# Optimization experiments

Measured on AMD Instinct MI355X. Metric: run time of the kernel, lower is better.

The kernel has to match this reference:

```python
import jax, jax.numpy as jnp
import numpy as np

N = 50000
E = 400000
IN_DIM = 16
EMB = 32
HID = 128
HEADS = 4
LAYERS = 3
EPS_BN = 1e-5
NEG_SLOPE = 0.2


def setup_inputs() -> dict:
    key = jax.random.key(0)
    ks = jax.random.split(key, 16)
    s = 0.1
    C = HID  # per-head out channels (concat=False)
    inp = {
        "x": jax.random.normal(ks[0], (N, IN_DIM), jnp.float32),
        "edge_index": jax.random.randint(ks[1], (2, E), 0, N, jnp.int64),
        "emb": s * jax.random.normal(ks[2], (N, EMB), jnp.float32),
        "Wf": s * jax.random.normal(ks[3], (EMB, IN_DIM), jnp.float32),
        "bf": jnp.zeros((EMB,), jnp.float32),
        "Wc": s * jax.random.normal(ks[4], (HID, 2 * EMB), jnp.float32),
        "bc": jnp.zeros((HID,), jnp.float32),
        "Wl": s * jax.random.normal(ks[5], (LAYERS, HEADS * C, HID), jnp.float32),
        "a_src": s * jax.random.normal(ks[6], (LAYERS, HEADS, C), jnp.float32),
        "a_dst": s * jax.random.normal(ks[7], (LAYERS, HEADS, C), jnp.float32),
        "bl": jnp.zeros((LAYERS, C), jnp.float32),
        "gamma": jnp.ones((LAYERS, C), jnp.float32),
        "beta": jnp.zeros((LAYERS, C), jnp.float32),
        "Wout": s * jax.random.normal(ks[8], (1, HID), jnp.float32),
        "bout": jnp.zeros((1,), jnp.float32),
    }
    return inp


def _gat_layer(h, src, dst, W, a_s, a_d, b):
    n = h.shape[0]
    C = W.shape[0] // HEADS
    hp = (h @ W.T).reshape(n, HEADS, C)                # (N,H,C)
    al_s = jnp.sum(hp * a_s, axis=-1)                  # (N,H)
    al_d = jnp.sum(hp * a_d, axis=-1)                  # (N,H)
    e = jax.nn.leaky_relu(al_s[src] + al_d[dst], NEG_SLOPE)  # (E,H)
    m = jax.ops.segment_max(e, dst, num_segments=n)    # per-target max
    ex = jnp.exp(e - m[dst])
    denom = jax.ops.segment_sum(ex, dst, num_segments=n) + 1e-16
    alpha = ex / denom[dst]                            # (E,H)
    msg = hp[src] * alpha[..., None]                   # (E,H,C)
    out = jax.ops.segment_sum(msg, dst, num_segments=n)
    return jnp.mean(out, axis=1) + b                   # concat=False: head mean


def _bn(x, g, b):
    mu = jnp.mean(x, axis=0)
    var = jnp.var(x, axis=0)  # biased, as torch BN uses for normalization
    return (x - mu) * jax.lax.rsqrt(var + EPS_BN) * g + b


def reference(x, edge_index, emb, Wf, bf, Wc, bc, Wl, a_src, a_dst, bl, gamma, beta, Wout, bout):
    n = x.shape[0]
    loop = jnp.arange(n, dtype=edge_index.dtype)
    src = jnp.concatenate([edge_index[0], loop])       # add self loops
    dst = jnp.concatenate([edge_index[1], loop])
    feat = x @ Wf.T + bf
    h = jax.nn.relu(jnp.concatenate([emb, feat], axis=1) @ Wc.T + bc)
    prev_h = h
    for i in range(LAYERS):
        h = _gat_layer(h, src, dst, Wl[i], a_src[i], a_dst[i], bl[i])
        h = jax.nn.relu(_bn(h, gamma[i], beta[i]))
        if prev_h.shape == h.shape:
            h = h + prev_h
        prev_h = h
    out = h @ Wout.T + bout
    return jnp.clip(out, -10.0, 10.0)
```

## Files before the change

kernel.cpp:

```cpp
#include <hip/hip_runtime.h>
#include <hip/hip_bf16.h>
#include <math.h>

#define INDIM 16
#define EMBD 32
#define UDIM 64
#define HIDD 128
#define HEADS 4
#define LAYERS 3
#define MPAD 50048
#define NSLICE 32

typedef short v8s __attribute__((ext_vector_type(8)));
typedef float v4f __attribute__((ext_vector_type(4)));

__device__ __forceinline__ float lrelu(float x) { return x > 0.f ? x : 0.2f * x; }
__device__ __forceinline__ float bf2f(unsigned int bits16) {
    unsigned int u = bits16 << 16;
    return __builtin_bit_cast(float, u);
}
__device__ __forceinline__ unsigned short f2bf(float f) {
    unsigned int u = __builtin_bit_cast(unsigned int, f);
    unsigned int lsb = (u >> 16) & 1;
    u += 0x7fff + lsb;
    return (unsigned short)(u >> 16);
}

__global__ __launch_bounds__(256) void k_enc(const float* __restrict__ x,
                                             const float* __restrict__ emb,
                                             const float* __restrict__ Wf,
                                             const float* __restrict__ bf,
                                             unsigned short* __restrict__ u, int n) {
    int i = blockIdx.x * 256 + threadIdx.x;
    if (i >= n * EMBD) return;
    int node = i >> 5, j = i & 31;
    const float* xr = x + (size_t)node * INDIM;
    const float* wr = Wf + (size_t)j * INDIM;
    float s = bf[j];
#pragma unroll
    for (int k = 0; k < INDIM; k++) s += xr[k] * wr[k];
    u[(size_t)node * UDIM + EMBD + j] = f2bf(s);
    u[(size_t)node * UDIM + j] = f2bf(emb[(size_t)node * EMBD + j]);
}

__global__ __launch_bounds__(256) void k_prep_v(const float* __restrict__ Wl,
                                                unsigned short* __restrict__ Vb) {
    int i = blockIdx.x * 256 + threadIdx.x;
    if (i >= LAYERS * HIDD * 512) return;
    int l = i >> 16;
    int rem = i & 65535;
    int c = rem >> 9;
    int f = rem & 511;
    int h = f >> 7, k = f & 127;
    Vb[i] = f2bf(Wl[(size_t)l * 512 * HIDD + (size_t)(h * HIDD + c) * HIDD + k]);
}

__global__ __launch_bounds__(256) void k_prep_a(const float* __restrict__ Wl,
                                                const float* __restrict__ a_s,
                                                const float* __restrict__ a_d,
                                                float* __restrict__ ws, float* __restrict__ wd) {
    int i = blockIdx.x * 256 + threadIdx.x;
    if (i >= LAYERS * HEADS * HIDD) return;
    int l = i >> 9, h = (i >> 7) & 3, k = i & 127;
    const float* W = Wl + (size_t)l * 512 * HIDD;
    const float* as = a_s + l * 512 + h * HIDD;
    const float* ad = a_d + l * 512 + h * HIDD;
    float ss = 0.f, sd = 0.f;
    for (int c = 0; c < HIDD; c++) {
        float w = W[(size_t)(h * HIDD + c) * HIDD + k];
        ss += as[c] * w;
        sd += ad[c] * w;
    }
    ws[i] = ss;
    wd[i] = sd;
}

__global__ __launch_bounds__(256) void k_prep_wc(const float* __restrict__ Wc,
                                                 unsigned short* __restrict__ Wcb) {
    int i = blockIdx.x * 256 + threadIdx.x;
    if (i < HIDD * UDIM) Wcb[i] = f2bf(Wc[i]);
}

__global__ __launch_bounds__(256) void k_gemm_enc(const unsigned short* __restrict__ A,
                                                  const unsigned short* __restrict__ B,
                                                  const float* __restrict__ bias,
                                                  float* __restrict__ O,
                                                  unsigned short* __restrict__ Ob, int M) {
    const int K = UDIM;
    int tid = threadIdx.x;
    int lane = tid & 63, wid = tid >> 6;
    int wm = wid >> 1, wn = wid & 1;
    int bm = blockIdx.x * 128;
    int lr = lane & 15, lk = lane >> 4;
    v4f acc[4][4] = {};
    const unsigned short* Abase = A + (size_t)(bm + wm * 64 + lr) * K + lk * 8;
    const unsigned short* Bbase = B + (size_t)(wn * 64 + lr) * K + lk * 8;
#pragma unroll
    for (int kk = 0; kk < K / 32; kk++) {
        v8s a[4], b[4];
#pragma unroll
        for (int f = 0; f < 4; f++) {
            a[f] = *(const v8s*)(Abase + (size_t)(f * 16) * K + kk * 32);
            b[f] = *(const v8s*)(Bbase + (size_t)(f * 16) * K + kk * 32);
        }
#pragma unroll
        for (int i = 0; i < 4; i++)
#pragma unroll
            for (int j = 0; j < 4; j++)
                acc[i][j] = __builtin_amdgcn_mfma_f32_16x16x32_bf16(a[i], b[j], acc[i][j], 0, 0, 0);
    }
#pragma unroll
    for (int i = 0; i < 4; i++) {
#pragma unroll
        for (int r = 0; r < 4; r++) {
            int row = bm + wm * 64 + i * 16 + lk * 4 + r;
            if (row >= M) continue;
#pragma unroll
            for (int j = 0; j < 4; j++) {
                int col = wn * 64 + j * 16 + lr;
                float v = fmaxf(acc[i][j][r] + bias[col], 0.f);
                O[(size_t)row * HIDD + col] = v;
                Ob[(size_t)row * HIDD + col] = f2bf(v);
            }
        }
    }
}

__global__ __launch_bounds__(256) void k_deg(const int* __restrict__ ei, int* __restrict__ deg,
                                             int E, int tot) {
    int e = blockIdx.x * 256 + threadIdx.x;
    if (e >= tot) return;
    int dst = (e < E) ? ei[E + e] : (e - E);
    atomicAdd(&deg[dst], 1);
}

__global__ __launch_bounds__(256) void k_scan1(const int* __restrict__ deg,
                                               int* __restrict__ rowptr,
                                               int* __restrict__ partials, int n) {
    int tid = threadIdx.x;
    int i = blockIdx.x * 256 + tid;
    int v = (i < n) ? deg[i] : 0;
    __shared__ int sm[256];
    sm[tid] = v;
    __syncthreads();
    for (int off = 1; off < 256; off <<= 1) {
        int t = (tid >= off) ? sm[tid - off] : 0;
        __syncthreads();
        sm[tid] += t;
        __syncthreads();
    }
    if (i < n) rowptr[i] = sm[tid] - v;
    if (tid == 255) partials[blockIdx.x] = sm[255];
}

__global__ __launch_bounds__(256) void k_scan2(int* __restrict__ partials, int nb) {
    int tid = threadIdx.x;
    int v = (tid < nb) ? partials[tid] : 0;
    __shared__ int sm[256];
    sm[tid] = v;
    __syncthreads();
    for (int off = 1; off < 256; off <<= 1) {
        int t = (tid >= off) ? sm[tid - off] : 0;
        __syncthreads();
        sm[tid] += t;
        __syncthreads();
    }
    if (tid < nb) partials[tid] = sm[tid] - v;
}

__global__ __launch_bounds__(256) void k_scan3(const int* __restrict__ deg,
                                               const int* __restrict__ partials,
                                               int* __restrict__ rowptr,
                                               int* __restrict__ cursor, int n) {
    int i = blockIdx.x * 256 + threadIdx.x;
    if (i >= n) return;
    int r = rowptr[i] + partials[blockIdx.x];
    rowptr[i] = r;
    cursor[i] = r;
    if (i == n - 1) rowptr[n] = r + deg[i];
}

__global__ __launch_bounds__(256) void k_scatter(const int* __restrict__ ei, int* __restrict__ cursor,
                                                 int* __restrict__ csr_src, int E, int tot) {
    int e = blockIdx.x * 256 + threadIdx.x;
    if (e >= tot) return;
    int src = (e < E) ? ei[e] : (e - E);
    int dst = (e < E) ? ei[E + e] : (e - E);
    int pos = atomicAdd(&cursor[dst], 1);
    csr_src[pos] = src;
}

__global__ __launch_bounds__(256) void k_al0(const float* __restrict__ h,
                                             const float* __restrict__ ws,
                                             const float* __restrict__ wd,
                                             float* __restrict__ al_s, float* __restrict__ al_d,
                                             int n) {
    int wid = threadIdx.x >> 6, lane = threadIdx.x & 63;
    int node = blockIdx.x * 4 + wid;
    if (node >= n) return;
    float2 v = *(const float2*)(h + (size_t)node * HIDD + 2 * lane);
    float s[8];
#pragma unroll
    for (int hh = 0; hh < 4; hh++) {
        float2 w1 = *(const float2*)(ws + hh * HIDD + 2 * lane);
        float2 w2 = *(const float2*)(wd + hh * HIDD + 2 * lane);
        s[hh] = v.x * w1.x + v.y * w1.y;
        s[4 + hh] = v.x * w2.x + v.y * w2.y;
    }
#pragma unroll
    for (int o = 32; o; o >>= 1)
#pragma unroll
        for (int q = 0; q < 8; q++) s[q] += __shfl_xor(s[q], o);
    if (lane == 0) {
        *(float4*)(al_s + (size_t)node * 4) = make_float4(s[0], s[1], s[2], s[3]);
        *(float4*)(al_d + (size_t)node * 4) = make_float4(s[4], s[5], s[6], s[7]);
    }
}

__global__ __launch_bounds__(1024) void k_layer(const int* __restrict__ rowptr,
                                                const int* __restrict__ csr_src,
                                                const float* __restrict__ al_s,
                                                const float* __restrict__ al_d,
                                                const unsigned short* __restrict__ hb,
                                                const unsigned short* __restrict__ Vb,
                                                float* __restrict__ agg,
                                                float* __restrict__ bns, int n) {
    __shared__ unsigned int Gw[16 * 256];
    __shared__ int Ssrc[16][64];
    __shared__ float Sal[16][4][64];
    int tid = threadIdx.x, lane = tid & 63, w = tid >> 6;
    int node0 = blockIdx.x * 16;
    int node = node0 + w;
    const float4* als4 = (const float4*)al_s;
    const unsigned int* h2 = (const unsigned int*)hb;
    int sw = (w & 7) << 2;

    if (node < n) {
        int start = rowptr[node], end = rowptr[node + 1];
        int deg = end - start;
        float4 ad = ((const float4*)al_d)[node];
        if (deg <= 64) {
            bool act = lane < deg;
            int src_l = act ? csr_src[start + lane] : 0;
            float e0 = -3.0e38f, e1 = -3.0e38f, e2 = -3.0e38f, e3 = -3.0e38f;
            if (act) {
                float4 as = als4[src_l];
                e0 = lrelu(as.x + ad.x);
                e1 = lrelu(as.y + ad.y);
                e2 = lrelu(as.z + ad.z);
                e3 = lrelu(as.w + ad.w);
            }
            int span = 1;
            while (span < deg) span <<= 1;
            float m0 = e0, m1 = e1, m2 = e2, m3 = e3;
            for (int o = 1; o < span; o <<= 1) {
                m0 = fmaxf(m0, __shfl_xor(m0, o));
                m1 = fmaxf(m1, __shfl_xor(m1, o));
                m2 = fmaxf(m2, __shfl_xor(m2, o));
                m3 = fmaxf(m3, __shfl_xor(m3, o));
            }
            float p0 = act ? expf(e0 - m0) : 0.f;
            float p1 = act ? expf(e1 - m1) : 0.f;
            float p2 = act ? expf(e2 - m2) : 0.f;
            float p3 = act ? expf(e3 - m3) : 0.f;
            float t0 = p0, t1 = p1, t2 = p2, t3 = p3;
            for (int o = 1; o < span; o <<= 1) {
                t0 += __shfl_xor(t0, o);
                t1 += __shfl_xor(t1, o);
                t2 += __shfl_xor(t2, o);
                t3 += __shfl_xor(t3, o);
            }
            Ssrc[w][lane] = src_l;
            Sal[w][0][lane] = p0 / (t0 + 1e-16f);
            Sal[w][1][lane] = p1 / (t1 + 1e-16f);
            Sal[w][2][lane] = p2 / (t2 + 1e-16f);
            Sal[w][3][lane] = p3 / (t3 + 1e-16f);

            float2 acc2[4] = {};
            for (int j0 = 0; j0 < deg; j0 += 8) {
                int4 sA = *(const int4*)&Ssrc[w][j0];
                int4 sB = *(const int4*)&Ssrc[w][j0 + 4];
                unsigned int u0 = h2[(size_t)sA.x * 64 + lane];
                unsigned int u1 = h2[(size_t)sA.y * 64 + lane];
                unsigned int u2 = h2[(size_t)sA.z * 64 + lane];
                unsigned int u3 = h2[(size_t)sA.w * 64 + lane];
                unsigned int u4 = h2[(size_t)sB.x * 64 + lane];
                unsigned int u5 = h2[(size_t)sB.y * 64 + lane];
                unsigned int u6 = h2[(size_t)sB.z * 64 + lane];
                unsigned int u7 = h2[(size_t)sB.w * 64 + lane];
                float4 a0A = *(const float4*)&Sal[w][0][j0];
                float4 a1A = *(const float4*)&Sal[w][1][j0];
                float4 a2A = *(const float4*)&Sal[w][2][j0];
                float4 a3A = *(const float4*)&Sal[w][3][j0];
                float4 a0B = *(const float4*)&Sal[w][0][j0 + 4];
                float4 a1B = *(const float4*)&Sal[w][1][j0 + 4];
                float4 a2B = *(const float4*)&Sal[w][2][j0 + 4];
                float4 a3B = *(const float4*)&Sal[w][3][j0 + 4];
#define EDGE_FMA(u, b0, b1, b2, b3)                                              \
    {                                                                            \
        float xlo = __builtin_bit_cast(float, (u) << 16);                        \
        float xhi = __builtin_bit_cast(float, (u) & 0xffff0000u);                \
        acc2[0].x = fmaf(b0, xlo, acc2[0].x);                                    \
        acc2[0].y = fmaf(b0, xhi, acc2[0].y);                                    \
        acc2[1].x = fmaf(b1, xlo, acc2[1].x);                                    \
        acc2[1].y = fmaf(b1, xhi, acc2[1].y);                                    \
        acc2[2].x = fmaf(b2, xlo, acc2[2].x);                                    \
        acc2[2].y = fmaf(b2, xhi, acc2[2].y);                                    \
        acc2[3].x = fmaf(b3, xlo, acc2[3].x);                                    \
        acc2[3].y = fmaf(b3, xhi, acc2[3].y);                                    \
    }
                EDGE_FMA(u0, a0A.x, a1A.x, a2A.x, a3A.x)
                EDGE_FMA(u1, a0A.y, a1A.y, a2A.y, a3A.y)
                EDGE_FMA(u2, a0A.z, a1A.z, a2A.z, a3A.z)
                EDGE_FMA(u3, a0A.w, a1A.w, a2A.w, a3A.w)
                EDGE_FMA(u4, a0B.x, a1B.x, a2B.x, a3B.x)
                EDGE_FMA(u5, a0B.y, a1B.y, a2B.y, a3B.y)
                EDGE_FMA(u6, a0B.z, a1B.z, a2B.z, a3B.z)
                EDGE_FMA(u7, a0B.w, a1B.w, a2B.w, a3B.w)
#undef EDGE_FMA
            }
#pragma unroll
            for (int hh = 0; hh < 4; hh++) {
                unsigned int p = (unsigned int)f2bf(acc2[hh].x) |
                                 ((unsigned int)f2bf(acc2[hh].y) << 16);
                Gw[w * 256 + ((hh * 64 + lane) ^ sw)] = p;
            }
        } else {
            float m0 = -3.0e38f, m1 = -3.0e38f, m2 = -3.0e38f, m3 = -3.0e38f;
            for (int j = start + lane; j < end; j += 64) {
                float4 as = als4[csr_src[j]];
                m0 = fmaxf(m0, lrelu(as.x + ad.x));
                m1 = fmaxf(m1, lrelu(as.y + ad.y));
                m2 = fmaxf(m2, lrelu(as.z + ad.z));
                m3 = fmaxf(m3, lrelu(as.w + ad.w));
            }
#pragma unroll
            for (int o = 32; o; o >>= 1) {
                m0 = fmaxf(m0, __shfl_xor(m0, o));
                m1 = fmaxf(m1, __shfl_xor(m1, o));
                m2 = fmaxf(m2, __shfl_xor(m2, o));
                m3 = fmaxf(m3, __shfl_xor(m3, o));
            }
            float t0 = 0.f, t1 = 0.f, t2 = 0.f, t3 = 0.f;
            for (int j = start + lane; j < end; j += 64) {
                float4 as = als4[csr_src[j]];
                t0 += expf(lrelu(as.x + ad.x) - m0);
                t1 += expf(lrelu(as.y + ad.y) - m1);
                t2 += expf(lrelu(as.z + ad.z) - m2);
                t3 += expf(lrelu(as.w + ad.w) - m3);
            }
#pragma unroll
            for (int o = 32; o; o >>= 1) {
                t0 += __shfl_xor(t0, o);
                t1 += __shfl_xor(t1, o);
                t2 += __shfl_xor(t2, o);
                t3 += __shfl_xor(t3, o);
            }
            float i0 = 1.f / (t0 + 1e-16f), i1 = 1.f / (t1 + 1e-16f);
            float i2 = 1.f / (t2 + 1e-16f), i3 = 1.f / (t3 + 1e-16f);
            float acc[4][2] = {};
            for (int base = start; base < end; base += 64) {
                int cnt = min(64, end - base);
                bool act2 = lane < cnt;
                int src_l = act2 ? csr_src[base + lane] : 0;
                float a0 = 0.f, a1 = 0.f, a2 = 0.f, a3 = 0.f;
                if (act2) {
                    float4 as = als4[src_l];
                    a0 = expf(lrelu(as.x + ad.x) - m0) * i0;
                    a1 = expf(lrelu(as.y + ad.y) - m1) * i1;
                    a2 = expf(lrelu(as.z + ad.z) - m2) * i2;
                    a3 = expf(lrelu(as.w + ad.w) - m3) * i3;
                }
                for (int jj = 0; jj < cnt; jj++) {
                    int sj = __shfl(src_l, jj);
                    float b0 = __shfl(a0, jj), b1 = __shfl(a1, jj);
                    float b2 = __shfl(a2, jj), b3 = __shfl(a3, jj);
                    unsigned int uu = h2[(size_t)sj * 64 + lane];
                    float x0 = bf2f(uu & 0xffff), x1 = bf2f(uu >> 16);
                    acc[0][0] += b0 * x0; acc[0][1] += b0 * x1;
                    acc[1][0] += b1 * x0; acc[1][1] += b1 * x1;
                    acc[2][0] += b2 * x0; acc[2][1] += b2 * x1;
                    acc[3][0] += b3 * x0; acc[3][1] += b3 * x1;
                }
            }
#pragma unroll
            for (int hh = 0; hh < 4; hh++) {
                unsigned int p = (unsigned int)f2bf(acc[hh][0]) |
                                 ((unsigned int)f2bf(acc[hh][1]) << 16);
                Gw[w * 256 + ((hh * 64 + lane) ^ sw)] = p;
            }
        }
    } else {
#pragma unroll
        for (int hh = 0; hh < 4; hh++) Gw[w * 256 + ((hh * 64 + lane) ^ sw)] = 0;
    }
    __syncthreads();

    if (w < 8) {
        int lr = lane & 15, lk = lane >> 4;
        int swr = (lr & 7) << 2;
        v4f a2 = {};
        const unsigned short* Bb = Vb + (size_t)(w * 16 + lr) * 512 + lk * 8;
#pragma unroll
        for (int kk = 0; kk < 16; kk++) {
            v8s a = *(const v8s*)(&Gw[lr * 256 + ((kk * 16 + lk * 4) ^ swr)]);
            v8s b = *(const v8s*)(Bb + kk * 32);
            a2 = __builtin_amdgcn_mfma_f32_16x16x32_bf16(a, b, a2, 0, 0, 0);
        }
        int col = w * 16 + lr;
        float ls = 0.f, lq = 0.f;
#pragma unroll
        for (int r = 0; r < 4; r++) {
            int nd = node0 + lk * 4 + r;
            float v = a2[r];
            if (nd < n) {
                agg[(size_t)nd * HIDD + col] = v;
                ls += v;
                lq += v * v;
            }
        }
        ls += __shfl_xor(ls, 16); lq += __shfl_xor(lq, 16);
        ls += __shfl_xor(ls, 32); lq += __shfl_xor(lq, 32);
        if (lk == 0) {
            float* slice = bns + (size_t)(blockIdx.x & (NSLICE - 1)) * 256;
            atomicAdd(&slice[col], ls);
            atomicAdd(&slice[128 + col], lq);
        }
    }
}

__global__ __launch_bounds__(128) void k_bnfin(const float* __restrict__ bns,
                                               const float* __restrict__ gamma,
                                               const float* __restrict__ beta,
                                               float* __restrict__ scale,
                                               float* __restrict__ shift, float invn) {
    int c = threadIdx.x;
    float s = 0.f, q = 0.f;
    for (int sl = 0; sl < NSLICE; sl++) {
        s += bns[sl * 256 + c];
        q += bns[sl * 256 + 128 + c];
    }
    float mu = s * invn;
    float var = q * invn - mu * mu;
    float sc = gamma[c] * rsqrtf(0.0625f * var + 1e-5f) * 0.25f;
    scale[c] = sc;
    shift[c] = beta[c] - mu * sc;
}

template <int MODE>
__global__ __launch_bounds__(256) void k_apply(const float* __restrict__ agg,
                                               const float* __restrict__ scale,
                                               const float* __restrict__ shift,
                                               float* __restrict__ h,
                                               unsigned short* __restrict__ hb,
                                               const float* __restrict__ ws,
                                               const float* __restrict__ wd,
                                               float* __restrict__ al_s,
                                               float* __restrict__ al_d,
                                               const float* __restrict__ Wout,
                                               const float* __restrict__ bout,
                                               float* __restrict__ out, int n) {
    int wid = threadIdx.x >> 6, lane = threadIdx.x & 63;
    int node = blockIdx.x * 4 + wid;
    if (node >= n) return;
    int c0 = 2 * lane, c1 = 2 * lane + 1;
    float2 ag = *(const float2*)(agg + (size_t)node * HIDD + c0);
    float2 ho = *(const float2*)(h + (size_t)node * HIDD + c0);
    float v0 = fmaxf(ag.x * scale[c0] + shift[c0], 0.f) + ho.x;
    float v1 = fmaxf(ag.y * scale[c1] + shift[c1], 0.f) + ho.y;
    if (MODE == 0) {
        *(float2*)(h + (size_t)node * HIDD + c0) = make_float2(v0, v1);
        ((unsigned int*)hb)[(size_t)node * 64 + lane] =
            (unsigned int)f2bf(v0) | ((unsigned int)f2bf(v1) << 16);
        float s[8];
#pragma unroll
        for (int hh = 0; hh < 4; hh++) {
            float2 w1 = *(const float2*)(ws + hh * HIDD + c0);
            float2 w2 = *(const float2*)(wd + hh * HIDD + c0);
            s[hh] = v0 * w1.x + v1 * w1.y;
            s[4 + hh] = v0 * w2.x + v1 * w2.y;
        }
#pragma unroll
        for (int o = 32; o; o >>= 1)
#pragma unroll
            for (int q = 0; q < 8; q++) s[q] += __shfl_xor(s[q], o);
        if (lane == 0) {
            *(float4*)(al_s + (size_t)node * 4) = make_float4(s[0], s[1], s[2], s[3]);
            *(float4*)(al_d + (size_t)node * 4) = make_float4(s[4], s[5], s[6], s[7]);
        }
    } else {
        float2 w = *(const float2*)(Wout + c0);
        float p = v0 * w.x + v1 * w.y;
#pragma unroll
        for (int o = 32; o; o >>= 1) p += __shfl_xor(p, o);
        if (lane == 0) {
            float v = p + bout[0];
            out[node] = fminf(fmaxf(v, -10.f), 10.f);
        }
    }
}

extern "C" void kernel_launch(void* const* d_in, const int* in_sizes, int n_in,
                              void* d_out, int out_size, void* d_ws, size_t ws_size,
                              hipStream_t stream) {
    const float* x = (const float*)d_in[0];
    const int* ei = (const int*)d_in[1];
    const float* emb = (const float*)d_in[2];
    const float* Wf = (const float*)d_in[3];
    const float* bf = (const float*)d_in[4];
    const float* Wc = (const float*)d_in[5];
    const float* bc = (const float*)d_in[6];
    const float* Wl = (const float*)d_in[7];
    const float* a_src = (const float*)d_in[8];
    const float* a_dst = (const float*)d_in[9];
    const float* gamma = (const float*)d_in[11];
    const float* beta = (const float*)d_in[12];
    const float* Wout = (const float*)d_in[13];
    const float* bout = (const float*)d_in[14];
    float* out = (float*)d_out;

    int n = in_sizes[0] / INDIM;
    int E = in_sizes[1] / 2;
    int tot = E + n;
    int NB = (n + 255) / 256;

    size_t off = 0;
    auto alloc = [&](size_t bytes) {
        void* p = (char*)d_ws + off;
        off = (off + bytes + 255) & ~(size_t)255;
        return p;
    };
    unsigned short* u = (unsigned short*)alloc((size_t)MPAD * UDIM * 2);
    float* h = (float*)alloc((size_t)MPAD * HIDD * 4);
    unsigned short* hb = (unsigned short*)alloc((size_t)MPAD * HIDD * 2);
    float* agg = (float*)alloc((size_t)MPAD * HIDD * 4);
    float* al_s = (float*)alloc((size_t)n * HEADS * 4);
    float* al_d = (float*)alloc((size_t)n * HEADS * 4);
    int* deg = (int*)alloc((size_t)n * 4);
    int* rowptr = (int*)alloc(((size_t)n + 1) * 4);
    int* cursor = (int*)alloc((size_t)n * 4);
    int* csr_src = (int*)alloc((size_t)tot * 4);
    int* partials = (int*)alloc((size_t)NB * 4);
    unsigned short* Vb = (unsigned short*)alloc((size_t)LAYERS * HIDD * 512 * 2);
    unsigned short* Wcb = (unsigned short*)alloc((size_t)HIDD * UDIM * 2);
    float* ws = (float*)alloc((size_t)LAYERS * HEADS * HIDD * 4);
    float* wd = (float*)alloc((size_t)LAYERS * HEADS * HIDD * 4);
    float* bnsums = (float*)alloc((size_t)LAYERS * NSLICE * 256 * 4);
    float* scale = (float*)alloc(128 * 4);
    float* shift = (float*)alloc(128 * 4);
    (void)ws_size;

    hipMemsetAsync(deg, 0, (size_t)n * 4, stream);
    hipMemsetAsync(bnsums, 0, (size_t)LAYERS * NSLICE * 256 * 4, stream);
    if (n < MPAD) {
        hipMemsetAsync(u + (size_t)n * UDIM, 0, (size_t)(MPAD - n) * UDIM * 2, stream);
    }

    k_prep_v<<<(LAYERS * HIDD * 512 + 255) / 256, 256, 0, stream>>>(Wl, Vb);
    k_prep_a<<<(LAYERS * HEADS * HIDD + 255) / 256, 256, 0, stream>>>(Wl, a_src, a_dst, ws, wd);
    k_prep_wc<<<(HIDD * UDIM + 255) / 256, 256, 0, stream>>>(Wc, Wcb);

    k_deg<<<(tot + 255) / 256, 256, 0, stream>>>(ei, deg, E, tot);
    k_scan1<<<NB, 256, 0, stream>>>(deg, rowptr, partials, n);
    k_scan2<<<1, 256, 0, stream>>>(partials, NB);
    k_scan3<<<NB, 256, 0, stream>>>(deg, partials, rowptr, cursor, n);
    k_scatter<<<(tot + 255) / 256, 256, 0, stream>>>(ei, cursor, csr_src, E, tot);

    k_enc<<<(n * EMBD + 255) / 256, 256, 0, stream>>>(x, emb, Wf, bf, u, n);
    k_gemm_enc<<<MPAD / 128, 256, 0, stream>>>(u, Wcb, bc, h, hb, n);
    k_al0<<<(n + 3) / 4, 256, 0, stream>>>(h, ws, wd, al_s, al_d, n);

    float invn = 1.0f / (float)n;
    int NLB = (n + 15) / 16;
    for (int l = 0; l < LAYERS; l++) {
        k_layer<<<NLB, 1024, 0, stream>>>(rowptr, csr_src, al_s, al_d, hb,
                                          Vb + (size_t)l * HIDD * 512, agg,
                                          bnsums + (size_t)l * NSLICE * 256, n);
        k_bnfin<<<1, 128, 0, stream>>>(bnsums + (size_t)l * NSLICE * 256, gamma + l * HIDD,
                                       beta + l * HIDD, scale, shift, invn);
        if (l < LAYERS - 1)
            k_apply<0><<<(n + 3) / 4, 256, 0, stream>>>(
                agg, scale, shift, h, hb,
                ws + (size_t)(l + 1) * 512, wd + (size_t)(l + 1) * 512, al_s, al_d,
                nullptr, nullptr, nullptr, n);
        else
            k_apply<1><<<(n + 3) / 4, 256, 0, stream>>>(
                agg, scale, shift, h, hb,
                nullptr, nullptr, nullptr, nullptr, Wout, bout, out, n);
    }
}
```

Before: 522.7 us.

## Store aggregates in bf16, prefetch gather loads, block-reduce BN stats, merge prep kernels

Several independent changes. The three weight-prep kernels become one launch, and the two memsets become one by placing bnsums right after deg. The layer kernel's gather loop switches from 8-wide batching to a 4-wide loop that prefetches the next group, which lowers register use. BN partial sums are reduced in shared memory before the global atomics. The aggregated output is now stored as bf16 instead of fp32, halving that write/read traffic at some precision cost in the BN input.

Result: faster. 457.4 us (-12.5%).

```diff
diff --git a/kernel.cpp b/kernel.cpp
--- a/kernel.cpp
+++ b/kernel.cpp
@@ -43,42 +43,41 @@
     u[(size_t)node * UDIM + j] = f2bf(emb[(size_t)node * EMBD + j]);
 }
 
-__global__ __launch_bounds__(256) void k_prep_v(const float* __restrict__ Wl,
-                                                unsigned short* __restrict__ Vb) {
+__global__ __launch_bounds__(256) void k_prep(const float* __restrict__ Wl,
+                                              const float* __restrict__ a_s,
+                                              const float* __restrict__ a_d,
+                                              const float* __restrict__ Wc,
+                                              unsigned short* __restrict__ Vb,
+                                              float* __restrict__ ws, float* __restrict__ wd,
+                                              unsigned short* __restrict__ Wcb) {
+    const int NV = LAYERS * HIDD * 512;
+    const int NA = LAYERS * HEADS * HIDD;
     int i = blockIdx.x * 256 + threadIdx.x;
-    if (i >= LAYERS * HIDD * 512) return;
-    int l = i >> 16;
-    int rem = i & 65535;
-    int c = rem >> 9;
-    int f = rem & 511;
-    int h = f >> 7, k = f & 127;
-    Vb[i] = f2bf(Wl[(size_t)l * 512 * HIDD + (size_t)(h * HIDD + c) * HIDD + k]);
-}
-
-__global__ __launch_bounds__(256) void k_prep_a(const float* __restrict__ Wl,
-                                                const float* __restrict__ a_s,
-                                                const float* __restrict__ a_d,
-                                                float* __restrict__ ws, float* __restrict__ wd) {
-    int i = blockIdx.x * 256 + threadIdx.x;
-    if (i >= LAYERS * HEADS * HIDD) return;
-    int l = i >> 9, h = (i >> 7) & 3, k = i & 127;
-    const float* W = Wl + (size_t)l * 512 * HIDD;
-    const float* as = a_s + l * 512 + h * HIDD;
-    const float* ad = a_d + l * 512 + h * HIDD;
-    float ss = 0.f, sd = 0.f;
-    for (int c = 0; c < HIDD; c++) {
-        float w = W[(size_t)(h * HIDD + c) * HIDD + k];
-        ss += as[c] * w;
-        sd += ad[c] * w;
-    }
-    ws[i] = ss;
-    wd[i] = sd;
-}
-
-__global__ __launch_bounds__(256) void k_prep_wc(const float* __restrict__ Wc,
-                                                 unsigned short* __restrict__ Wcb) {
-    int i = blockIdx.x * 256 + threadIdx.x;
-    if (i < HIDD * UDIM) Wcb[i] = f2bf(Wc[i]);
+    if (i < NV) {
+        int l = i >> 16;
+        int rem = i & 65535;
+        int c = rem >> 9;
+        int f = rem & 511;
+        int h = f >> 7, k = f & 127;
+        Vb[i] = f2bf(Wl[(size_t)l * 512 * HIDD + (size_t)(h * HIDD + c) * HIDD + k]);
+    } else if (i < NV + NA) {
+        int j = i - NV;
+        int l = j >> 9, h = (j >> 7) & 3, k = j & 127;
+        const float* W = Wl + (size_t)l * 512 * HIDD;
+        const float* as = a_s + l * 512 + h * HIDD;
+        const float* ad = a_d + l * 512 + h * HIDD;
+        float ss = 0.f, sd = 0.f;
+        for (int c = 0; c < HIDD; c++) {
+            float w = W[(size_t)(h * HIDD + c) * HIDD + k];
+            ss += as[c] * w;
+            sd += ad[c] * w;
+        }
+        ws[j] = ss;
+        wd[j] = sd;
+    } else if (i < NV + NA + HIDD * UDIM) {
+        int j = i - NV - NA;
+        Wcb[j] = f2bf(Wc[j]);
+    }
 }
 
 __global__ __launch_bounds__(256) void k_gemm_enc(const unsigned short* __restrict__ A,
@@ -223,12 +222,14 @@
                                                 const float* __restrict__ al_d,
                                                 const unsigned short* __restrict__ hb,
                                                 const unsigned short* __restrict__ Vb,
-                                                float* __restrict__ agg,
+                                                unsigned short* __restrict__ aggb,
                                                 float* __restrict__ bns, int n) {
     __shared__ unsigned int Gw[16 * 256];
+    __shared__ float s1[128], s2[128];
     __shared__ int Ssrc[16][64];
     __shared__ float Sal[16][4][64];
     int tid = threadIdx.x, lane = tid & 63, w = tid >> 6;
+    if (tid < 128) { s1[tid] = 0.f; s2[tid] = 0.f; }
     int node0 = blockIdx.x * 16;
     int node = node0 + w;
     const float4* als4 = (const float4*)al_s;
@@ -277,25 +278,25 @@
             Sal[w][3][lane] = p3 / (t3 + 1e-16f);
 
             float2 acc2[4] = {};
-            for (int j0 = 0; j0 < deg; j0 += 8) {
-                int4 sA = *(const int4*)&Ssrc[w][j0];
-                int4 sB = *(const int4*)&Ssrc[w][j0 + 4];
-                unsigned int u0 = h2[(size_t)sA.x * 64 + lane];
-                unsigned int u1 = h2[(size_t)sA.y * 64 + lane];
-                unsigned int u2 = h2[(size_t)sA.z * 64 + lane];
-                unsigned int u3 = h2[(size_t)sA.w * 64 + lane];
-                unsigned int u4 = h2[(size_t)sB.x * 64 + lane];
-                unsigned int u5 = h2[(size_t)sB.y * 64 + lane];
-                unsigned int u6 = h2[(size_t)sB.z * 64 + lane];
-                unsigned int u7 = h2[(size_t)sB.w * 64 + lane];
-                float4 a0A = *(const float4*)&Sal[w][0][j0];
-                float4 a1A = *(const float4*)&Sal[w][1][j0];
-                float4 a2A = *(const float4*)&Sal[w][2][j0];
-                float4 a3A = *(const float4*)&Sal[w][3][j0];
-                float4 a0B = *(const float4*)&Sal[w][0][j0 + 4];
-                float4 a1B = *(const float4*)&Sal[w][1][j0 + 4];
-                float4 a2B = *(const float4*)&Sal[w][2][j0 + 4];
-                float4 a3B = *(const float4*)&Sal[w][3][j0 + 4];
+            int4 sC = *(const int4*)&Ssrc[w][0];
+            unsigned int c0 = h2[(size_t)sC.x * 64 + lane];
+            unsigned int c1 = h2[(size_t)sC.y * 64 + lane];
+            unsigned int c2 = h2[(size_t)sC.z * 64 + lane];
+            unsigned int c3 = h2[(size_t)sC.w * 64 + lane];
+            for (int j0 = 0; j0 < deg; j0 += 4) {
+                unsigned int n0 = 0, n1 = 0, n2 = 0, n3 = 0;
+                int jn = j0 + 4;
+                if (jn < deg) {
+                    int4 sN = *(const int4*)&Ssrc[w][jn];
+                    n0 = h2[(size_t)sN.x * 64 + lane];
+                    n1 = h2[(size_t)sN.y * 64 + lane];
+                    n2 = h2[(size_t)sN.z * 64 + lane];
+                    n3 = h2[(size_t)sN.w * 64 + lane];
+                }
+                float4 a0 = *(const float4*)&Sal[w][0][j0];
+                float4 a1 = *(const float4*)&Sal[w][1][j0];
+                float4 a2 = *(const float4*)&Sal[w][2][j0];
+                float4 a3 = *(const float4*)&Sal[w][3][j0];
 #define EDGE_FMA(u, b0, b1, b2, b3)                                              \
     {                                                                            \
         float xlo = __builtin_bit_cast(float, (u) << 16);                        \
@@ -309,15 +310,12 @@
         acc2[3].x = fmaf(b3, xlo, acc2[3].x);                                    \
         acc2[3].y = fmaf(b3, xhi, acc2[3].y);                                    \
     }
-                EDGE_FMA(u0, a0A.x, a1A.x, a2A.x, a3A.x)
-                EDGE_FMA(u1, a0A.y, a1A.y, a2A.y, a3A.y)
-                EDGE_FMA(u2, a0A.z, a1A.z, a2A.z, a3A.z)
-                EDGE_FMA(u3, a0A.w, a1A.w, a2A.w, a3A.w)
-                EDGE_FMA(u4, a0B.x, a1B.x, a2B.x, a3B.x)
-                EDGE_FMA(u5, a0B.y, a1B.y, a2B.y, a3B.y)
-                EDGE_FMA(u6, a0B.z, a1B.z, a2B.z, a3B.z)
-                EDGE_FMA(u7, a0B.w, a1B.w, a2B.w, a3B.w)
+                EDGE_FMA(c0, a0.x, a1.x, a2.x, a3.x)
+                EDGE_FMA(c1, a0.y, a1.y, a2.y, a3.y)
+                EDGE_FMA(c2, a0.z, a1.z, a2.z, a3.z)
+                EDGE_FMA(c3, a0.w, a1.w, a2.w, a3.w)
 #undef EDGE_FMA
+                c0 = n0; c1 = n1; c2 = n2; c3 = n3;
             }
 #pragma unroll
             for (int hh = 0; hh < 4; hh++) {
@@ -414,18 +412,19 @@
             int nd = node0 + lk * 4 + r;
             float v = a2[r];
             if (nd < n) {
-                agg[(size_t)nd * HIDD + col] = v;
+                aggb[(size_t)nd * HIDD + col] = f2bf(v);
                 ls += v;
                 lq += v * v;
             }
         }
-        ls += __shfl_xor(ls, 16); lq += __shfl_xor(lq, 16);
-        ls += __shfl_xor(ls, 32); lq += __shfl_xor(lq, 32);
-        if (lk == 0) {
-            float* slice = bns + (size_t)(blockIdx.x & (NSLICE - 1)) * 256;
-            atomicAdd(&slice[col], ls);
-            atomicAdd(&slice[128 + col], lq);
-        }
+        atomicAdd(&s1[col], ls);
+        atomicAdd(&s2[col], lq);
+    }
+    __syncthreads();
+    if (tid < 128) {
+        float* slice = bns + (size_t)(blockIdx.x & (NSLICE - 1)) * 256;
+        atomicAdd(&slice[tid], s1[tid]);
+        atomicAdd(&slice[128 + tid], s2[tid]);
     }
 }
 
@@ -448,7 +447,7 @@
 }
 
 template <int MODE>
-__global__ __launch_bounds__(256) void k_apply(const float* __restrict__ agg,
+__global__ __launch_bounds__(256) void k_apply(const unsigned short* __restrict__ aggb,
                                                const float* __restrict__ scale,
                                                const float* __restrict__ shift,
                                                float* __restrict__ h,
@@ -464,10 +463,11 @@
     int node = blockIdx.x * 4 + wid;
     if (node >= n) return;
     int c0 = 2 * lane, c1 = 2 * lane + 1;
-    float2 ag = *(const float2*)(agg + (size_t)node * HIDD + c0);
+    unsigned int ag2 = ((const unsigned int*)aggb)[(size_t)node * 64 + lane];
+    float agx = bf2f(ag2 & 0xffff), agy = bf2f(ag2 >> 16);
     float2 ho = *(const float2*)(h + (size_t)node * HIDD + c0);
-    float v0 = fmaxf(ag.x * scale[c0] + shift[c0], 0.f) + ho.x;
-    float v1 = fmaxf(ag.y * scale[c1] + shift[c1], 0.f) + ho.y;
+    float v0 = fmaxf(agx * scale[c0] + shift[c0], 0.f) + ho.x;
+    float v1 = fmaxf(agy * scale[c1] + shift[c1], 0.f) + ho.y;
     if (MODE == 0) {
         *(float2*)(h + (size_t)node * HIDD + c0) = make_float2(v0, v1);
         ((unsigned int*)hb)[(size_t)node * 64 + lane] =
@@ -533,10 +533,11 @@
     unsigned short* u = (unsigned short*)alloc((size_t)MPAD * UDIM * 2);
     float* h = (float*)alloc((size_t)MPAD * HIDD * 4);
     unsigned short* hb = (unsigned short*)alloc((size_t)MPAD * HIDD * 2);
-    float* agg = (float*)alloc((size_t)MPAD * HIDD * 4);
+    unsigned short* aggb = (unsigned short*)alloc((size_t)MPAD * HIDD * 2);
     float* al_s = (float*)alloc((size_t)n * HEADS * 4);
     float* al_d = (float*)alloc((size_t)n * HEADS * 4);
     int* deg = (int*)alloc((size_t)n * 4);
+    float* bnsums = (float*)alloc((size_t)LAYERS * NSLICE * 256 * 4);
     int* rowptr = (int*)alloc(((size_t)n + 1) * 4);
     int* cursor = (int*)alloc((size_t)n * 4);
     int* csr_src = (int*)alloc((size_t)tot * 4);
@@ -545,20 +546,19 @@
     unsigned short* Wcb = (unsigned short*)alloc((size_t)HIDD * UDIM * 2);
     float* ws = (float*)alloc((size_t)LAYERS * HEADS * HIDD * 4);
     float* wd = (float*)alloc((size_t)LAYERS * HEADS * HIDD * 4);
-    float* bnsums = (float*)alloc((size_t)LAYERS * NSLICE * 256 * 4);
     float* scale = (float*)alloc(128 * 4);
     float* shift = (float*)alloc(128 * 4);
     (void)ws_size;
 
-    hipMemsetAsync(deg, 0, (size_t)n * 4, stream);
-    hipMemsetAsync(bnsums, 0, (size_t)LAYERS * NSLICE * 256 * 4, stream);
+    hipMemsetAsync(deg, 0, (char*)(bnsums + LAYERS * NSLICE * 256) - (char*)deg, stream);
     if (n < MPAD) {
         hipMemsetAsync(u + (size_t)n * UDIM, 0, (size_t)(MPAD - n) * UDIM * 2, stream);
     }
 
-    k_prep_v<<<(LAYERS * HIDD * 512 + 255) / 256, 256, 0, stream>>>(Wl, Vb);
-    k_prep_a<<<(LAYERS * HEADS * HIDD + 255) / 256, 256, 0, stream>>>(Wl, a_src, a_dst, ws, wd);
-    k_prep_wc<<<(HIDD * UDIM + 255) / 256, 256, 0, stream>>>(Wc, Wcb);
+    {
+        int total = LAYERS * HIDD * 512 + LAYERS * HEADS * HIDD + HIDD * UDIM;
+        k_prep<<<(total + 255) / 256, 256, 0, stream>>>(Wl, a_src, a_dst, Wc, Vb, ws, wd, Wcb);
+    }
 
     k_deg<<<(tot + 255) / 256, 256, 0, stream>>>(ei, deg, E, tot);
     k_scan1<<<NB, 256, 0, stream>>>(deg, rowptr, partials, n);
@@ -574,18 +574,18 @@
     int NLB = (n + 15) / 16;
     for (int l = 0; l < LAYERS; l++) {
         k_layer<<<NLB, 1024, 0, stream>>>(rowptr, csr_src, al_s, al_d, hb,
-                                          Vb + (size_t)l * HIDD * 512, agg,
+                                          Vb + (size_t)l * HIDD * 512, aggb,
                                           bnsums + (size_t)l * NSLICE * 256, n);
         k_bnfin<<<1, 128, 0, stream>>>(bnsums + (size_t)l * NSLICE * 256, gamma + l * HIDD,
                                        beta + l * HIDD, scale, shift, invn);
         if (l < LAYERS - 1)
             k_apply<0><<<(n + 3) / 4, 256, 0, stream>>>(
-                agg, scale, shift, h, hb,
+                aggb, scale, shift, h, hb,
                 ws + (size_t)(l + 1) * 512, wd + (size_t)(l + 1) * 512, al_s, al_d,
                 nullptr, nullptr, nullptr, n);
         else
             k_apply<1><<<(n + 3) / 4, 256, 0, stream>>>(
-                agg, scale, shift, h, hb,
+                aggb, scale, shift, h, hb,
                 nullptr, nullptr, nullptr, nullptr, Wout, bout, out, n);
     }
 }
```
